# Kernel optimization log

Measured on AMD Instinct MI355X. Metric: run time of the kernel, lower is better.

The kernel has to match this reference:

```python
import jax, jax.numpy as jnp
import numpy as np

H = 8        # heads
DH = 64      # dim_head
EPS = 1e-5   # LayerNorm eps (torch default)


def setup_inputs() -> dict:
    key = jax.random.key(0)
    k0, k1, k2, k3, k4 = jax.random.split(key, 5)
    b, l, n, dim = 2, 8, 256, 512
    inner = H * DH
    return {
        "xyzs": jax.random.normal(k0, (b, l, n, 3), dtype=jnp.float32),
        "features": jax.random.normal(k1, (b, l, n, dim), dtype=jnp.float32),
        "ln_gamma": jnp.ones((dim,), dtype=jnp.float32),
        "ln_beta": jnp.zeros((dim,), dtype=jnp.float32),
        "w_qkv": jax.random.normal(k2, (dim, 3 * inner), dtype=jnp.float32) * 0.02,
        "w_sp": jax.random.normal(k3, (3, DH), dtype=jnp.float32) * 0.3,
        "w_out": jax.random.normal(k4, (inner, dim), dtype=jnp.float32) * 0.02,
        "b_out": jnp.zeros((dim,), dtype=jnp.float32),
    }


def reference(xyzs, features, ln_gamma, ln_beta, w_qkv, w_sp, w_out, b_out):
    b, l, n, dim = features.shape
    m = l * n
    inner = H * DH
    scale = DH ** (-0.5)

    # LayerNorm over last dim (biased variance, eps=1e-5)
    mu = jnp.mean(features, axis=-1, keepdims=True)
    var = jnp.var(features, axis=-1, keepdims=True)
    normed = (features - mu) * jax.lax.rsqrt(var + EPS) * ln_gamma + ln_beta

    # qkv projection, chunk into q,k,v, reshape 'b l n (h d) -> b h (l n) d'
    qkv = normed.reshape(b, m, dim) @ w_qkv            # [b, m, 3*inner]
    def split_heads(t):
        return t.reshape(b, m, H, DH).transpose(0, 2, 1, 3)  # [b, h, m, d]
    q = split_heads(qkv[..., :inner])
    k = split_heads(qkv[..., inner:2 * inner])
    v = split_heads(qkv[..., 2 * inner:])

    dots = jnp.einsum('bhid,bhjd->bhij', q, k) * scale  # [b, h, m, m]
    attn = jax.nn.softmax(dots, axis=-1)
    v_out = jnp.einsum('bhij,bhjd->bhid', attn, v)      # [b, h, m, d]

    # pairwise coordinate deltas: delta[b,i,j,c] = xyz[b,j,c] - xyz[b,i,c]
    xyz_f = xyzs.reshape(b, m, 3)
    delta = xyz_f[:, None, :, :] - xyz_f[:, :, None, :]  # [b, m, m, 3]
    # attention-weighted aggregation over j (avoids [b,h,m,m,3] intermediate)
    agg = jnp.einsum('bhij,bijc->bhic', attn, delta)     # [b, h, m, 3]
    disp = agg @ w_sp                                    # [b, h, m, DH]

    out = v_out + disp                                   # [b, h, m, DH]
    out = out.transpose(0, 2, 1, 3).reshape(b, m, inner) # 'b h m d -> b m (h d)'
    out = jax.nn.gelu(out @ w_out + b_out, approximate=False)
    return out.reshape(b, l, n, dim) + features
```

## Files before the change

kernel.cpp:

```cpp
#include <hip/hip_runtime.h>
#include <hip/hip_bf16.h>
#include <math.h>

#define BB   2
#define MM   2048
#define DIM  512
#define NH   8
#define DHd  64
#define NQK  1536
#define ROWS 4096

typedef __hip_bfloat16 bf16;
typedef __attribute__((ext_vector_type(8))) short bf16x8;
typedef __attribute__((ext_vector_type(4))) float f32x4;
typedef __attribute__((ext_vector_type(16))) float f32x16;
typedef __attribute__((ext_vector_type(8))) unsigned short us8;
typedef __attribute__((ext_vector_type(4))) unsigned int u32x4;

__device__ __forceinline__ unsigned short f2bf_bits(float x) {
    bf16 h = __float2bfloat16(x);
    return *(unsigned short*)&h;
}
__device__ __forceinline__ float bf2f(unsigned short u) {
    unsigned int v = ((unsigned int)u) << 16;
    return __uint_as_float(v);
}
__device__ __forceinline__ unsigned cvtpk_bf16(float lo, float hi) {
    unsigned r;
    asm("v_cvt_pk_bf16_f32 %0, %1, %2" : "=v"(r) : "v"(lo), "v"(hi));
    return r;
}
__device__ __forceinline__ void pl32swap(unsigned &a, unsigned &b) {
    asm volatile("v_permlane32_swap_b32 %0, %1" : "+v"(a), "+v"(b));
}

__global__ __launch_bounds__(256) void pre_kernel(
    const float* __restrict__ feat, const float* __restrict__ gamma,
    const float* __restrict__ beta, unsigned short* __restrict__ normed,
    const float* __restrict__ wqkv, const float* __restrict__ wout,
    unsigned short* __restrict__ wqkvT, unsigned short* __restrict__ woutT)
{
    __shared__ float st[64][65];
    int b = blockIdx.x;
    int tid = threadIdx.x;
    if (b < ROWS / 4) {
        int w = tid >> 6, lane = tid & 63;
        int row = b * 4 + w;
        const float* fr = feat + (size_t)row * DIM + lane * 8;
        float4 v0 = *(const float4*)fr;
        float4 v1 = *(const float4*)(fr + 4);
        float s  = v0.x + v0.y + v0.z + v0.w + v1.x + v1.y + v1.z + v1.w;
        float ss = v0.x*v0.x + v0.y*v0.y + v0.z*v0.z + v0.w*v0.w
                 + v1.x*v1.x + v1.y*v1.y + v1.z*v1.z + v1.w*v1.w;
        #pragma unroll
        for (int o = 32; o >= 1; o >>= 1) { s += __shfl_xor(s, o); ss += __shfl_xor(ss, o); }
        float mu  = s * (1.0f / DIM);
        float var = ss * (1.0f / DIM) - mu * mu;
        float inv = rsqrtf(var + 1e-5f);
        const float* gp = gamma + lane * 8;
        const float* bp = beta  + lane * 8;
        float4 g0 = *(const float4*)gp, g1 = *(const float4*)(gp + 4);
        float4 e0 = *(const float4*)bp, e1 = *(const float4*)(bp + 4);
        unsigned short ov[8];
        ov[0] = f2bf_bits((v0.x - mu) * inv * g0.x + e0.x);
        ov[1] = f2bf_bits((v0.y - mu) * inv * g0.y + e0.y);
        ov[2] = f2bf_bits((v0.z - mu) * inv * g0.z + e0.z);
        ov[3] = f2bf_bits((v0.w - mu) * inv * g0.w + e0.w);
        ov[4] = f2bf_bits((v1.x - mu) * inv * g1.x + e1.x);
        ov[5] = f2bf_bits((v1.y - mu) * inv * g1.y + e1.y);
        ov[6] = f2bf_bits((v1.z - mu) * inv * g1.z + e1.z);
        ov[7] = f2bf_bits((v1.w - mu) * inv * g1.w + e1.w);
        *(us8*)&normed[(size_t)row * DIM + lane * 8] = *(us8*)ov;
        return;
    }
    int idx = b - ROWS / 4;
    const float* in; unsigned short* out; int N, n0;
    if (idx < 192) { in = wqkv; out = wqkvT; N = NQK; n0 = (idx >> 3) * 64; }
    else { idx -= 192; in = wout; out = woutT; N = DIM; n0 = (idx >> 3) * 64; }
    int k0 = (idx & 7) * 64;
    #pragma unroll
    for (int p = 0; p < 16; p++) {
        int e = tid + p * 256;
        int r = e >> 6, c = e & 63;
        st[r][c] = in[(size_t)(k0 + r) * N + n0 + c];
    }
    __syncthreads();
    #pragma unroll
    for (int p = 0; p < 16; p++) {
        int e = tid + p * 256;
        int nr = e >> 6, kc = e & 63;
        out[(size_t)(n0 + nr) * DIM + k0 + kc] = f2bf_bits(st[kc][nr]);
    }
}

__global__ __launch_bounds__(256) void qkv_gemm(
    const unsigned short* __restrict__ A, const unsigned short* __restrict__ BT,
    unsigned short* __restrict__ qd, unsigned short* __restrict__ kd,
    unsigned short* __restrict__ vd)
{
    __shared__ __align__(16) unsigned short sA[128 * 72];
    __shared__ __align__(16) unsigned short sB[64 * 72];
    int tid = threadIdx.x;
    int r0 = blockIdx.x * 128;
    int n0 = blockIdx.y * 64;
    int chunk = n0 >> 9;
    int h     = (n0 & 511) >> 6;
    int w = tid >> 6, lane = tid & 63;
    int wm = w >> 1, wn = w & 1;
    int ln15 = lane & 15, quad = lane >> 4;

    int arow = tid >> 1, acol = (tid & 1) * 32;
    int brow = tid >> 2, bcol = (tid & 3) * 16;

    f32x4 acc[4][2] = {};
    us8 ra[4], rb[2];

    #pragma unroll
    for (int u = 0; u < 4; u++)
        ra[u] = *(const us8*)&A[(size_t)(r0 + arow) * DIM + acol + u * 8];
    #pragma unroll
    for (int u = 0; u < 2; u++)
        rb[u] = *(const us8*)&BT[(size_t)(n0 + brow) * DIM + bcol + u * 8];

    for (int k0 = 0; k0 < DIM; k0 += 64) {
        __syncthreads();
        #pragma unroll
        for (int u = 0; u < 4; u++) *(us8*)&sA[arow * 72 + acol + u * 8] = ra[u];
        #pragma unroll
        for (int u = 0; u < 2; u++) *(us8*)&sB[brow * 72 + bcol + u * 8] = rb[u];
        __syncthreads();
        int kn = k0 + 64;
        if (kn < DIM) {
            #pragma unroll
            for (int u = 0; u < 4; u++)
                ra[u] = *(const us8*)&A[(size_t)(r0 + arow) * DIM + kn + acol + u * 8];
            #pragma unroll
            for (int u = 0; u < 2; u++)
                rb[u] = *(const us8*)&BT[(size_t)(n0 + brow) * DIM + kn + bcol + u * 8];
        }
        bf16x8 fa[4][2], fb[2][2];
        #pragma unroll
        for (int i = 0; i < 4; i++)
            #pragma unroll
            for (int kk = 0; kk < 2; kk++)
                fa[i][kk] = *(const bf16x8*)&sA[(wm * 64 + i * 16 + ln15) * 72 + kk * 32 + quad * 8];
        #pragma unroll
        for (int j = 0; j < 2; j++)
            #pragma unroll
            for (int kk = 0; kk < 2; kk++)
                fb[j][kk] = *(const bf16x8*)&sB[(wn * 32 + j * 16 + ln15) * 72 + kk * 32 + quad * 8];
        if (chunk == 2) {
            #pragma unroll
            for (int kk = 0; kk < 2; kk++)
                #pragma unroll
                for (int i = 0; i < 4; i++)
                    #pragma unroll
                    for (int j = 0; j < 2; j++)
                        acc[i][j] = __builtin_amdgcn_mfma_f32_16x16x32_bf16(fa[i][kk], fb[j][kk], acc[i][j], 0, 0, 0);
        } else {
            #pragma unroll
            for (int kk = 0; kk < 2; kk++)
                #pragma unroll
                for (int i = 0; i < 4; i++)
                    #pragma unroll
                    for (int j = 0; j < 2; j++)
                        acc[i][j] = __builtin_amdgcn_mfma_f32_16x16x32_bf16(fb[j][kk], fa[i][kk], acc[i][j], 0, 0, 0);
        }
    }

    if (chunk == 2) {
        #pragma unroll
        for (int i = 0; i < 4; i++) {
            int gm = r0 + wm * 64 + i * 16 + quad * 4;
            int bb = gm >> 11, mm = gm & 2047;
            #pragma unroll
            for (int j = 0; j < 2; j++) {
                int d = wn * 32 + j * 16 + ln15;
                ushort4 pk;
                pk.x = f2bf_bits(acc[i][j][0]);
                pk.y = f2bf_bits(acc[i][j][1]);
                pk.z = f2bf_bits(acc[i][j][2]);
                pk.w = f2bf_bits(acc[i][j][3]);
                *(ushort4*)&vd[((size_t)(bb * NH + h) * DHd + d) * MM + mm] = pk;
            }
        }
    } else {
        unsigned short* dst = (chunk == 0) ? qd : kd;
        float sc = (chunk == 0) ? 0.125f : 1.0f;
        #pragma unroll
        for (int i = 0; i < 4; i++) {
            int gm = r0 + wm * 64 + i * 16 + ln15;
            int bb = gm >> 11, mm = gm & 2047;
            #pragma unroll
            for (int j = 0; j < 2; j++) {
                int d0 = wn * 32 + j * 16 + quad * 4;
                ushort4 pk;
                pk.x = f2bf_bits(acc[i][j][0] * sc);
                pk.y = f2bf_bits(acc[i][j][1] * sc);
                pk.z = f2bf_bits(acc[i][j][2] * sc);
                pk.w = f2bf_bits(acc[i][j][3] * sc);
                *(ushort4*)&dst[((size_t)(bb * NH + h) * MM + mm) * DHd + d0] = pk;
            }
        }
    }
}

__global__ __launch_bounds__(128, 1) void attn_kernel(
    const unsigned short* __restrict__ qg, const unsigned short* __restrict__ kg,
    const unsigned short* __restrict__ vg, const float* __restrict__ xyzs,
    const float* __restrict__ wsp, unsigned short* __restrict__ attn_out)
{
    __shared__ __align__(16) unsigned short sK[64 * 72];
    __shared__ __align__(16) unsigned short sVT[96 * 72];
    __shared__ float sW[3][64];

    int tid = threadIdx.x;
    int bh = blockIdx.y; int bb = bh >> 3; int hh = bh & 7;
    int i0 = blockIdx.x * 64;
    int w = tid >> 6;
    int lane = tid & 63;
    int ln31 = lane & 31;
    int hi   = lane >> 5;
    int hi8  = hi * 8;

    for (int e = tid; e < 28 * 72; e += 128) sVT[68 * 72 + e] = 0;
    if (tid < 64) sVT[67 * 72 + tid] = 0x3F80;
    for (int e = tid; e < 192; e += 128) sW[e >> 6][e & 63] = wsp[e];

    bf16x8 aq[4];
    {
        const unsigned short* q0 = qg + ((size_t)bh * MM + i0 + w * 32 + ln31) * DHd + hi8;
        #pragma unroll
        for (int kc = 0; kc < 4; kc++)
            aq[kc] = *(const bf16x8*)(q0 + kc * 16);
    }

    f32x16 ot[3] = {};

    const unsigned short* kbase = kg + (size_t)bh * MM * DHd;
    const unsigned short* vbase = vg + (size_t)bh * DHd * MM;

    int srow = tid >> 1, scolB = (tid & 1) * 32;
    int key0 = tid / 3, c0 = tid - key0 * 3;
    int e1 = tid + 128;
    int key1 = e1 / 3, c1 = e1 - key1 * 3;

    us8 rk[4], rv[4];
    float rx0 = 0.f, rx1 = 0.f;
    {
        const unsigned short* ks = kbase + (size_t)srow * DHd + scolB;
        const unsigned short* vs = vbase + (size_t)srow * MM + scolB;
        #pragma unroll
        for (int u = 0; u < 4; u++) {
            rk[u] = *(const us8*)(ks + u * 8);
            rv[u] = *(const us8*)(vs + u * 8);
        }
        rx0 = xyzs[(size_t)bb * MM * 3 + tid];
        if (tid < 64) rx1 = xyzs[(size_t)bb * MM * 3 + e1];
    }

    for (int jt = 0; jt < MM; jt += 64) {
        __syncthreads();
        #pragma unroll
        for (int u = 0; u < 4; u++) {
            *(us8*)&sK[srow * 72 + scolB + u * 8]  = rk[u];
            *(us8*)&sVT[srow * 72 + scolB + u * 8] = rv[u];
        }
        sVT[(64 + c0) * 72 + key0] = f2bf_bits(rx0);
        if (tid < 64) sVT[(64 + c1) * 72 + key1] = f2bf_bits(rx1);
        __syncthreads();
        int jn = jt + 64;
        if (jn < MM) {
            const unsigned short* ks = kbase + (size_t)(jn + srow) * DHd + scolB;
            const unsigned short* vs = vbase + (size_t)srow * MM + jn + scolB;
            #pragma unroll
            for (int u = 0; u < 4; u++) {
                rk[u] = *(const us8*)(ks + u * 8);
                rv[u] = *(const us8*)(vs + u * 8);
            }
            rx0 = xyzs[((size_t)bb * MM + jn) * 3 + tid];
            if (tid < 64) rx1 = xyzs[((size_t)bb * MM + jn) * 3 + e1];
        }

        #pragma unroll
        for (int b = 0; b < 2; b++) {
            f32x16 zz = {};
            #pragma unroll
            for (int kc = 0; kc < 4; kc++) {
                bf16x8 kf = *(const bf16x8*)&sK[(b * 32 + ln31) * 72 + kc * 16 + hi8];
                zz = __builtin_amdgcn_mfma_f32_32x32x16_bf16(kf, aq[kc], zz, 0, 0, 0);
            }
            unsigned c_[8];
            #pragma unroll
            for (int j = 0; j < 8; j++)
                c_[j] = cvtpk_bf16(__expf(zz[2 * j]), __expf(zz[2 * j + 1]));
            unsigned x0 = c_[0], x2 = c_[2]; pl32swap(x0, x2);
            unsigned x1 = c_[1], x3 = c_[3]; pl32swap(x1, x3);
            unsigned y0 = c_[4], y2 = c_[6]; pl32swap(y0, y2);
            unsigned y1 = c_[5], y3 = c_[7]; pl32swap(y1, y3);
            u32x4 xv = {x0, x1, x2, x3};
            u32x4 yv = {y0, y1, y2, y3};
            bf16x8 X = *(bf16x8*)&xv;
            bf16x8 Y = *(bf16x8*)&yv;
            #pragma unroll
            for (int vb = 0; vb < 3; vb++) {
                bf16x8 v0 = *(const bf16x8*)&sVT[(vb * 32 + ln31) * 72 + b * 32 + hi8];
                bf16x8 v1 = *(const bf16x8*)&sVT[(vb * 32 + ln31) * 72 + b * 32 + 16 + hi8];
                ot[vb] = __builtin_amdgcn_mfma_f32_32x32x16_bf16(v0, X, ot[vb], 0, 0, 0);
                ot[vb] = __builtin_amdgcn_mfma_f32_32x32x16_bf16(v1, Y, ot[vb], 0, 0, 0);
            }
        }
    }

    int gq = i0 + w * 32 + ln31;
    float invl = 1.f / __shfl(ot[2][3], ln31);
    size_t xb = ((size_t)bb * MM + gq) * 3;
    float gx = __shfl(ot[2][0], ln31) * invl - xyzs[xb + 0];
    float gy = __shfl(ot[2][1], ln31) * invl - xyzs[xb + 1];
    float gz = __shfl(ot[2][2], ln31) * invl - xyzs[xb + 2];
    unsigned short* dst = attn_out + ((size_t)bb * MM + gq) * DIM + hh * DHd;
    #pragma unroll
    for (int vb = 0; vb < 2; vb++) {
        #pragma unroll
        for (int rq = 0; rq < 4; rq++) {
            int d0 = vb * 32 + rq * 8 + hi * 4;
            ushort4 pk;
            #pragma unroll
            for (int j = 0; j < 4; j++) {
                int d = d0 + j;
                float v = ot[vb][rq * 4 + j] * invl
                        + gx * sW[0][d] + gy * sW[1][d] + gz * sW[2][d];
                ((unsigned short*)&pk)[j] = f2bf_bits(v);
            }
            *(ushort4*)&dst[d0] = pk;
        }
    }
}

__global__ __launch_bounds__(256) void out_gemm(
    const unsigned short* __restrict__ A, const unsigned short* __restrict__ BT,
    const float* __restrict__ bias, const float* __restrict__ feat,
    float* __restrict__ out)
{
    __shared__ __align__(16) unsigned short sA[64 * 72];
    __shared__ __align__(16) unsigned short sB[64 * 72];
    int tid = threadIdx.x;
    int r0 = blockIdx.x * 64, n0 = blockIdx.y * 64;
    int w = tid >> 6, lane = tid & 63;
    int wm = w >> 1, wn = w & 1;
    int ln15 = lane & 15, quad = lane >> 4;

    int srow = tid >> 2, scol = (tid & 3) * 16;

    f32x4 acc[2][2] = {};
    us8 ra[2], rb[2];

    #pragma unroll
    for (int u = 0; u < 2; u++) {
        ra[u] = *(const us8*)&A[(size_t)(r0 + srow) * DIM + scol + u * 8];
        rb[u] = *(const us8*)&BT[(size_t)(n0 + srow) * DIM + scol + u * 8];
    }

    for (int k0 = 0; k0 < DIM; k0 += 64) {
        __syncthreads();
        #pragma unroll
        for (int u = 0; u < 2; u++) {
            *(us8*)&sA[srow * 72 + scol + u * 8] = ra[u];
            *(us8*)&sB[srow * 72 + scol + u * 8] = rb[u];
        }
        __syncthreads();
        int kn = k0 + 64;
        if (kn < DIM) {
            #pragma unroll
            for (int u = 0; u < 2; u++) {
                ra[u] = *(const us8*)&A[(size_t)(r0 + srow) * DIM + kn + scol + u * 8];
                rb[u] = *(const us8*)&BT[(size_t)(n0 + srow) * DIM + kn + scol + u * 8];
            }
        }
        bf16x8 af[2][2], bf_[2][2];
        #pragma unroll
        for (int i = 0; i < 2; i++)
            #pragma unroll
            for (int kk = 0; kk < 2; kk++)
                af[i][kk] = *(const bf16x8*)&sA[(wm * 32 + i * 16 + ln15) * 72 + kk * 32 + quad * 8];
        #pragma unroll
        for (int j = 0; j < 2; j++)
            #pragma unroll
            for (int kk = 0; kk < 2; kk++)
                bf_[j][kk] = *(const bf16x8*)&sB[(wn * 32 + j * 16 + ln15) * 72 + kk * 32 + quad * 8];
        #pragma unroll
        for (int kk = 0; kk < 2; kk++)
            #pragma unroll
            for (int i = 0; i < 2; i++)
                #pragma unroll
                for (int j = 0; j < 2; j++)
                    acc[i][j] = __builtin_amdgcn_mfma_f32_16x16x32_bf16(af[i][kk], bf_[j][kk], acc[i][j], 0, 0, 0);
    }

    #pragma unroll
    for (int i = 0; i < 2; i++) {
        #pragma unroll
        for (int reg = 0; reg < 4; reg++) {
            int gr = r0 + wm * 32 + i * 16 + quad * 4 + reg;
            #pragma unroll
            for (int j = 0; j < 2; j++) {
                int c = n0 + wn * 32 + j * 16 + ln15;
                float x = acc[i][j][reg] + bias[c];
                float g = 0.5f * x * (1.f + erff(x * 0.70710678118f));
                out[(size_t)gr * DIM + c] = g + feat[(size_t)gr * DIM + c];
            }
        }
    }
}

extern "C" void kernel_launch(void* const* d_in, const int* in_sizes, int n_in,
                              void* d_out, int out_size, void* d_ws, size_t ws_size,
                              hipStream_t stream)
{
    const float* xyzs  = (const float*)d_in[0];
    const float* feat  = (const float*)d_in[1];
    const float* gamma = (const float*)d_in[2];
    const float* beta  = (const float*)d_in[3];
    const float* wqkv  = (const float*)d_in[4];
    const float* wsp   = (const float*)d_in[5];
    const float* wout  = (const float*)d_in[6];
    const float* bout  = (const float*)d_in[7];
    float* out = (float*)d_out;

    unsigned short* ws16 = (unsigned short*)d_ws;
    const size_t SEGS = (size_t)ROWS * DIM;
    unsigned short* normed = ws16;
    unsigned short* qb     = ws16 + SEGS;
    unsigned short* kb     = ws16 + 2 * SEGS;
    unsigned short* vb     = ws16 + 3 * SEGS;
    unsigned short* wqkvT  = ws16 + 4 * SEGS;
    unsigned short* woutT  = wqkvT + (size_t)NQK * DIM;

    pre_kernel<<<ROWS / 4 + 256, 256, 0, stream>>>(feat, gamma, beta, normed,
                                                   wqkv, wout, wqkvT, woutT);
    qkv_gemm<<<dim3(32, 24), 256, 0, stream>>>(normed, wqkvT, qb, kb, vb);
    attn_kernel<<<dim3(32, 16), 128, 0, stream>>>(qb, kb, vb, xyzs, wsp, normed);
    out_gemm<<<dim3(64, 8), 256, 0, stream>>>(normed, woutT, bout, feat, out);
}
```

Baseline: 154.6 us.

## Split attention key range across three wave groups with shared-memory reduction

The attention block grows from 128 to 384 threads. Three pairs of waves each process about a third of the key sequence with their own shared K/V buffers, and the partial output accumulators are summed through shared memory before normalization and the xyz displacement epilogue. Separately, the log2(e) factor is folded into the q scale so the kernel can use exp2f instead of __expf. The goal is more waves per CU and more latency hiding for the 512-block grid, at the cost of extra shared memory, block-wide syncs and a reduction step.

```diff
diff --git a/kernel.cpp b/kernel.cpp
--- a/kernel.cpp
+++ b/kernel.cpp
@@ -186,7 +186,7 @@
         }
     } else {
         unsigned short* dst = (chunk == 0) ? qd : kd;
-        float sc = (chunk == 0) ? 0.125f : 1.0f;
+        float sc = (chunk == 0) ? 0.18033688f : 1.0f;
         #pragma unroll
         for (int i = 0; i < 4; i++) {
             int gm = r0 + wm * 64 + i * 16 + ln15;
@@ -205,31 +205,39 @@
     }
 }
 
-__global__ __launch_bounds__(128, 1) void attn_kernel(
+__global__ __launch_bounds__(384, 3) void attn_kernel(
     const unsigned short* __restrict__ qg, const unsigned short* __restrict__ kg,
     const unsigned short* __restrict__ vg, const float* __restrict__ xyzs,
     const float* __restrict__ wsp, unsigned short* __restrict__ attn_out)
 {
-    __shared__ __align__(16) unsigned short sK[64 * 72];
-    __shared__ __align__(16) unsigned short sVT[96 * 72];
+    __shared__ __align__(16) unsigned short sAll[3 * 160 * 72];
     __shared__ float sW[3][64];
 
     int tid = threadIdx.x;
     int bh = blockIdx.y; int bb = bh >> 3; int hh = bh & 7;
     int i0 = blockIdx.x * 64;
-    int w = tid >> 6;
+    int wid = tid >> 6;
     int lane = tid & 63;
+    int qf   = wid & 1;
+    int ksid = wid >> 1;
     int ln31 = lane & 31;
     int hi   = lane >> 5;
     int hi8  = hi * 8;
 
-    for (int e = tid; e < 28 * 72; e += 128) sVT[68 * 72 + e] = 0;
-    if (tid < 64) sVT[67 * 72 + tid] = 0x3F80;
-    for (int e = tid; e < 192; e += 128) sW[e >> 6][e & 63] = wsp[e];
+    unsigned short* sK  = &sAll[ksid * 160 * 72];
+    unsigned short* sVT = sK + 64 * 72;
+
+    int g = tid & 127;
+    int jbeg = ksid * 704;
+    int jend = (ksid == 2) ? MM : jbeg + 704;
+
+    for (int e = g; e < 28 * 72; e += 128) sVT[68 * 72 + e] = 0;
+    if (g < 64) sVT[67 * 72 + g] = 0x3F80;
+    for (int e = tid; e < 192; e += 384) sW[e >> 6][e & 63] = wsp[e];
 
     bf16x8 aq[4];
     {
-        const unsigned short* q0 = qg + ((size_t)bh * MM + i0 + w * 32 + ln31) * DHd + hi8;
+        const unsigned short* q0 = qg + ((size_t)bh * MM + i0 + qf * 32 + ln31) * DHd + hi8;
         #pragma unroll
         for (int kc = 0; kc < 4; kc++)
             aq[kc] = *(const bf16x8*)(q0 + kc * 16);
@@ -240,99 +248,130 @@
     const unsigned short* kbase = kg + (size_t)bh * MM * DHd;
     const unsigned short* vbase = vg + (size_t)bh * DHd * MM;
 
-    int srow = tid >> 1, scolB = (tid & 1) * 32;
-    int key0 = tid / 3, c0 = tid - key0 * 3;
-    int e1 = tid + 128;
+    int srow = g >> 1, scolB = (g & 1) * 32;
+    int key0 = g / 3, c0 = g - key0 * 3;
+    int e1 = g + 128;
     int key1 = e1 / 3, c1 = e1 - key1 * 3;
 
     us8 rk[4], rv[4];
     float rx0 = 0.f, rx1 = 0.f;
     {
-        const unsigned short* ks = kbase + (size_t)srow * DHd + scolB;
-        const unsigned short* vs = vbase + (size_t)srow * MM + scolB;
+        const unsigned short* ksrc = kbase + (size_t)(jbeg + srow) * DHd + scolB;
+        const unsigned short* vsrc = vbase + (size_t)srow * MM + jbeg + scolB;
         #pragma unroll
         for (int u = 0; u < 4; u++) {
-            rk[u] = *(const us8*)(ks + u * 8);
-            rv[u] = *(const us8*)(vs + u * 8);
-        }
-        rx0 = xyzs[(size_t)bb * MM * 3 + tid];
-        if (tid < 64) rx1 = xyzs[(size_t)bb * MM * 3 + e1];
-    }
-
-    for (int jt = 0; jt < MM; jt += 64) {
-        __syncthreads();
-        #pragma unroll
-        for (int u = 0; u < 4; u++) {
-            *(us8*)&sK[srow * 72 + scolB + u * 8]  = rk[u];
-            *(us8*)&sVT[srow * 72 + scolB + u * 8] = rv[u];
-        }
-        sVT[(64 + c0) * 72 + key0] = f2bf_bits(rx0);
-        if (tid < 64) sVT[(64 + c1) * 72 + key1] = f2bf_bits(rx1);
+            rk[u] = *(const us8*)(ksrc + u * 8);
+            rv[u] = *(const us8*)(vsrc + u * 8);
+        }
+        rx0 = xyzs[((size_t)bb * MM + jbeg) * 3 + g];
+        if (g < 64) rx1 = xyzs[((size_t)bb * MM + jbeg) * 3 + e1];
+    }
+
+    for (int t = 0; t < 11; ++t) {
+        int jt = jbeg + t * 64;
+        bool act = jt < jend;
+        __syncthreads();
+        if (act) {
+            #pragma unroll
+            for (int u = 0; u < 4; u++) {
+                *(us8*)&sK[srow * 72 + scolB + u * 8]  = rk[u];
+                *(us8*)&sVT[srow * 72 + scolB + u * 8] = rv[u];
+            }
+            sVT[(64 + c0) * 72 + key0] = f2bf_bits(rx0);
+            if (g < 64) sVT[(64 + c1) * 72 + key1] = f2bf_bits(rx1);
+        }
         __syncthreads();
         int jn = jt + 64;
-        if (jn < MM) {
-            const unsigned short* ks = kbase + (size_t)(jn + srow) * DHd + scolB;
-            const unsigned short* vs = vbase + (size_t)srow * MM + jn + scolB;
+        if (jn < jend) {
+            const unsigned short* ksrc = kbase + (size_t)(jn + srow) * DHd + scolB;
+            const unsigned short* vsrc = vbase + (size_t)srow * MM + jn + scolB;
             #pragma unroll
             for (int u = 0; u < 4; u++) {
-                rk[u] = *(const us8*)(ks + u * 8);
-                rv[u] = *(const us8*)(vs + u * 8);
-            }
-            rx0 = xyzs[((size_t)bb * MM + jn) * 3 + tid];
-            if (tid < 64) rx1 = xyzs[((size_t)bb * MM + jn) * 3 + e1];
-        }
-
-        #pragma unroll
-        for (int b = 0; b < 2; b++) {
-            f32x16 zz = {};
-            #pragma unroll
-            for (int kc = 0; kc < 4; kc++) {
-                bf16x8 kf = *(const bf16x8*)&sK[(b * 32 + ln31) * 72 + kc * 16 + hi8];
-                zz = __builtin_amdgcn_mfma_f32_32x32x16_bf16(kf, aq[kc], zz, 0, 0, 0);
-            }
-            unsigned c_[8];
-            #pragma unroll
-            for (int j = 0; j < 8; j++)
-                c_[j] = cvtpk_bf16(__expf(zz[2 * j]), __expf(zz[2 * j + 1]));
-            unsigned x0 = c_[0], x2 = c_[2]; pl32swap(x0, x2);
-            unsigned x1 = c_[1], x3 = c_[3]; pl32swap(x1, x3);
-            unsigned y0 = c_[4], y2 = c_[6]; pl32swap(y0, y2);
-            unsigned y1 = c_[5], y3 = c_[7]; pl32swap(y1, y3);
-            u32x4 xv = {x0, x1, x2, x3};
-            u32x4 yv = {y0, y1, y2, y3};
-            bf16x8 X = *(bf16x8*)&xv;
-            bf16x8 Y = *(bf16x8*)&yv;
-            #pragma unroll
-            for (int vb = 0; vb < 3; vb++) {
-                bf16x8 v0 = *(const bf16x8*)&sVT[(vb * 32 + ln31) * 72 + b * 32 + hi8];
-                bf16x8 v1 = *(const bf16x8*)&sVT[(vb * 32 + ln31) * 72 + b * 32 + 16 + hi8];
-                ot[vb] = __builtin_amdgcn_mfma_f32_32x32x16_bf16(v0, X, ot[vb], 0, 0, 0);
-                ot[vb] = __builtin_amdgcn_mfma_f32_32x32x16_bf16(v1, Y, ot[vb], 0, 0, 0);
-            }
-        }
-    }
-
-    int gq = i0 + w * 32 + ln31;
-    float invl = 1.f / __shfl(ot[2][3], ln31);
-    size_t xb = ((size_t)bb * MM + gq) * 3;
-    float gx = __shfl(ot[2][0], ln31) * invl - xyzs[xb + 0];
-    float gy = __shfl(ot[2][1], ln31) * invl - xyzs[xb + 1];
-    float gz = __shfl(ot[2][2], ln31) * invl - xyzs[xb + 2];
-    unsigned short* dst = attn_out + ((size_t)bb * MM + gq) * DIM + hh * DHd;
-    #pragma unroll
-    for (int vb = 0; vb < 2; vb++) {
-        #pragma unroll
-        for (int rq = 0; rq < 4; rq++) {
-            int d0 = vb * 32 + rq * 8 + hi * 4;
-            ushort4 pk;
-            #pragma unroll
-            for (int j = 0; j < 4; j++) {
-                int d = d0 + j;
-                float v = ot[vb][rq * 4 + j] * invl
-                        + gx * sW[0][d] + gy * sW[1][d] + gz * sW[2][d];
-                ((unsigned short*)&pk)[j] = f2bf_bits(v);
-            }
-            *(ushort4*)&dst[d0] = pk;
+                rk[u] = *(const us8*)(ksrc + u * 8);
+                rv[u] = *(const us8*)(vsrc + u * 8);
+            }
+            rx0 = xyzs[((size_t)bb * MM + jn) * 3 + g];
+            if (g < 64) rx1 = xyzs[((size_t)bb * MM + jn) * 3 + e1];
+        }
+        if (act) {
+            #pragma unroll
+            for (int b = 0; b < 2; b++) {
+                f32x16 zz = {};
+                #pragma unroll
+                for (int kc = 0; kc < 4; kc++) {
+                    bf16x8 kf = *(const bf16x8*)&sK[(b * 32 + ln31) * 72 + kc * 16 + hi8];
+                    zz = __builtin_amdgcn_mfma_f32_32x32x16_bf16(kf, aq[kc], zz, 0, 0, 0);
+                }
+                unsigned c_[8];
+                #pragma unroll
+                for (int j = 0; j < 8; j++)
+                    c_[j] = cvtpk_bf16(exp2f(zz[2 * j]), exp2f(zz[2 * j + 1]));
+                unsigned x0 = c_[0], x2 = c_[2]; pl32swap(x0, x2);
+                unsigned x1 = c_[1], x3 = c_[3]; pl32swap(x1, x3);
+                unsigned y0 = c_[4], y2 = c_[6]; pl32swap(y0, y2);
+                unsigned y1 = c_[5], y3 = c_[7]; pl32swap(y1, y3);
+                u32x4 xv = {x0, x1, x2, x3};
+                u32x4 yv = {y0, y1, y2, y3};
+                bf16x8 X = *(bf16x8*)&xv;
+                bf16x8 Y = *(bf16x8*)&yv;
+                #pragma unroll
+                for (int vb = 0; vb < 3; vb++) {
+                    bf16x8 v0 = *(const bf16x8*)&sVT[(vb * 32 + ln31) * 72 + b * 32 + hi8];
+                    bf16x8 v1 = *(const bf16x8*)&sVT[(vb * 32 + ln31) * 72 + b * 32 + 16 + hi8];
+                    ot[vb] = __builtin_amdgcn_mfma_f32_32x32x16_bf16(v0, X, ot[vb], 0, 0, 0);
+                    ot[vb] = __builtin_amdgcn_mfma_f32_32x32x16_bf16(v1, Y, ot[vb], 0, 0, 0);
+                }
+            }
+        }
+    }
+
+    __syncthreads();
+    float* red = (float*)sAll;
+    if (ksid >= 1) {
+        float* dst = red + (((ksid - 1) * 2 + qf) * 64 + lane) * 52;
+        #pragma unroll
+        for (int vb = 0; vb < 3; vb++) {
+            #pragma unroll
+            for (int r = 0; r < 4; r++) {
+                f32x4 tq = {ot[vb][r * 4 + 0], ot[vb][r * 4 + 1],
+                            ot[vb][r * 4 + 2], ot[vb][r * 4 + 3]};
+                *(f32x4*)&dst[vb * 16 + r * 4] = tq;
+            }
+        }
+    }
+    __syncthreads();
+    if (ksid == 0) {
+        #pragma unroll
+        for (int part = 0; part < 2; part++) {
+            const float* src = red + ((part * 2 + qf) * 64 + lane) * 52;
+            #pragma unroll
+            for (int vb = 0; vb < 3; vb++)
+                #pragma unroll
+                for (int j = 0; j < 16; j++)
+                    ot[vb][j] += src[vb * 16 + j];
+        }
+        int gq = i0 + qf * 32 + ln31;
+        float invl = 1.f / __shfl(ot[2][3], ln31);
+        size_t xb = ((size_t)bb * MM + gq) * 3;
+        float gx = __shfl(ot[2][0], ln31) * invl - xyzs[xb + 0];
+        float gy = __shfl(ot[2][1], ln31) * invl - xyzs[xb + 1];
+        float gz = __shfl(ot[2][2], ln31) * invl - xyzs[xb + 2];
+        unsigned short* dst = attn_out + ((size_t)bb * MM + gq) * DIM + hh * DHd;
+        #pragma unroll
+        for (int vb = 0; vb < 2; vb++) {
+            #pragma unroll
+            for (int rq = 0; rq < 4; rq++) {
+                int d0 = vb * 32 + rq * 8 + hi * 4;
+                ushort4 pk;
+                #pragma unroll
+                for (int j = 0; j < 4; j++) {
+                    int d = d0 + j;
+                    float v = ot[vb][rq * 4 + j] * invl
+                            + gx * sW[0][d] + gy * sW[1][d] + gz * sW[2][d];
+                    ((unsigned short*)&pk)[j] = f2bf_bits(v);
+                }
+                *(ushort4*)&dst[d0] = pk;
+            }
         }
     }
 }
@@ -439,6 +478,6 @@
     pre_kernel<<<ROWS / 4 + 256, 256, 0, stream>>>(feat, gamma, beta, normed,
                                                    wqkv, wout, wqkvT, woutT);
     qkv_gemm<<<dim3(32, 24), 256, 0, stream>>>(normed, wqkvT, qb, kb, vb);
-    attn_kernel<<<dim3(32, 16), 128, 0, stream>>>(qb, kb, vb, xyzs, wsp, normed);
+    attn_kernel<<<dim3(32, 16), 384, 0, stream>>>(qb, kb, vb, xyzs, wsp, normed);
     out_gemm<<<dim3(64, 8), 256, 0, stream>>>(normed, woutT, bout, feat, out);
 }
```

Result: slower. 162.5 us (+5.1%).
